# Kernel optimization log

Hardware: AMD Instinct MI355X
Metric: run time of the kernel (lower is better)

The kernel has to match this reference:

```python
import jax, jax.numpy as jnp
import numpy as np

E = 32      # feature/query dim
H = 4       # heads
HD = E // H # head dim = 8
N_LAYERS = 12
N_Q = 16
B = 128
S = 512


def _mha(q, kv, Wqkv, bqkv, Wo, bo):
    # PyTorch nn.MultiheadAttention (batch_first), eval mode (no dropout).
    Wq, Wk, Wv = jnp.split(Wqkv, 3, axis=0)   # each [E, E]
    bq, bk, bv = jnp.split(bqkv, 3)

    def heads(x, W, b):
        y = x @ W.T + b                         # [B, L, E]
        b_, l_, _ = y.shape
        return y.reshape(b_, l_, H, HD).transpose(0, 2, 1, 3)  # [B, H, L, HD]

    qh, kh, vh = heads(q, Wq, bq), heads(kv, Wk, bk), heads(kv, Wv, bv)
    scores = jnp.einsum('bhqd,bhkd->bhqk', qh, kh) / np.sqrt(HD).astype(np.float32)
    att = jax.nn.softmax(scores, axis=-1)
    o = jnp.einsum('bhqk,bhkd->bhqd', att, vh)
    o = o.transpose(0, 2, 1, 3).reshape(q.shape[0], q.shape[1], E)
    return o @ Wo.T + bo


def setup_inputs() -> dict:
    key = jax.random.key(0)
    ks = iter(jax.random.split(key, 64))
    g = lambda shape, s=0.05: (jax.random.normal(next(ks), shape, dtype=jnp.float32) * s)
    inp = {
        'x_omic': jax.random.normal(next(ks), (B, 80), dtype=jnp.float32),
        'x_path': jax.random.normal(next(ks), (B, S, E), dtype=jnp.float32),
        # frozen omic FFN encoder: 80 -> 64 -> 48 -> 32 -> 32, ELU each
        'omic_W0': g((64, 80)), 'omic_b0': g((64,)),
        'omic_W1': g((48, 64)), 'omic_b1': g((48,)),
        'omic_W2': g((32, 48)), 'omic_b2': g((32,)),
        'omic_W3': g((E, 32)),  'omic_b3': g((E,)),
        'ln_g': jnp.ones((E,), jnp.float32), 'ln_b': jnp.zeros((E,), jnp.float32),
        'corr_Wqkv': g((3 * E, E)), 'corr_bqkv': g((3 * E,)),
        'corr_Wo': g((E, E)), 'corr_bo': g((E,)),
        # 12 stacked query<->omic and query<->path cross-attentions
        'qo_Wqkv': g((N_LAYERS, 3 * E, E)), 'qo_bqkv': g((N_LAYERS, 3 * E)),
        'qo_Wo': g((N_LAYERS, E, E)), 'qo_bo': g((N_LAYERS, E)),
        'qp_Wqkv': g((N_LAYERS, 3 * E, E)), 'qp_bqkv': g((N_LAYERS, 3 * E)),
        'qp_Wo': g((N_LAYERS, E, E)), 'qp_bo': g((N_LAYERS, E)),
        # 12 stacked 2-layer FFNs (Linear-ReLU-Linear, no residual in source)
        'ffn_W1': g((N_LAYERS, E, E)), 'ffn_b1': g((N_LAYERS, E)),
        'ffn_W2': g((N_LAYERS, E, E)), 'ffn_b2': g((N_LAYERS, E)),
        'Qs': jax.random.normal(next(ks), (N_Q, E), dtype=jnp.float32),
        'grade_W': g((3, E)), 'grade_b': g((3,)),
        'haz_W': g((1, E)), 'haz_b': g((1,)),
    }
    return inp


def reference(x_omic, x_path, omic_W0, omic_b0, omic_W1, omic_b1, omic_W2, omic_b2,
              omic_W3, omic_b3, ln_g, ln_b, corr_Wqkv, corr_bqkv, corr_Wo, corr_bo,
              qo_Wqkv, qo_bqkv, qo_Wo, qo_bo, qp_Wqkv, qp_bqkv, qp_Wo, qp_bo,
              ffn_W1, ffn_b1, ffn_W2, ffn_b2, Qs, grade_W, grade_b, haz_W, haz_b):
    # frozen omic encoder (eval mode: AlphaDropout is identity)
    h = jax.nn.elu(x_omic @ omic_W0.T + omic_b0)
    h = jax.nn.elu(h @ omic_W1.T + omic_b1)
    h = jax.nn.elu(h @ omic_W2.T + omic_b2)
    omic_emb = jax.nn.elu(h @ omic_W3.T + omic_b3)[:, None, :]   # [B, 1, E]

    qs = jnp.broadcast_to(Qs[None], (x_omic.shape[0], N_Q, E))    # [B, 16, E]

    # correlation self-attention on LayerNorm(x_path), residual on raw x_path
    mu = jnp.mean(x_path, axis=-1, keepdims=True)
    var = jnp.var(x_path, axis=-1, keepdims=True)
    xn = (x_path - mu) / jnp.sqrt(var + 1e-5) * ln_g + ln_b
    img = x_path + _mha(xn, xn, corr_Wqkv, corr_bqkv, corr_Wo, corr_bo)

    for i in range(N_LAYERS):
        qs = _mha(qs, omic_emb, qo_Wqkv[i], qo_bqkv[i], qo_Wo[i], qo_bo[i])
        qs = _mha(qs, img, qp_Wqkv[i], qp_bqkv[i], qp_Wo[i], qp_bo[i])
        qs = jax.nn.relu(qs @ ffn_W1[i].T + ffn_b1[i]) @ ffn_W2[i].T + ffn_b2[i]

    features = qs.mean(axis=1)                                    # [B, E]
    grade = jax.nn.log_softmax(features @ grade_W.T + grade_b, axis=1)
    hazard = jax.nn.sigmoid(features @ haz_W.T + haz_b) * 6.0 - 3.0
    return features, grade, hazard
```

## Files before the change

### kernel.cpp

```cpp
#include <hip/hip_runtime.h>
#include <hip/hip_bf16.h>

typedef __attribute__((ext_vector_type(8))) short short8;
typedef __attribute__((ext_vector_type(4))) float f32x4;

__device__ __forceinline__ float elu1(float x) { return x > 0.f ? x : expm1f(x); }
__device__ __forceinline__ unsigned pkbf(float a, float b) {
  return (unsigned)__bfloat16_as_ushort(__float2bfloat16(a)) |
         ((unsigned)__bfloat16_as_ushort(__float2bfloat16(b)) << 16);
}
__device__ __forceinline__ short8 cvt8(float4 a, float4 b, float s) {
  uint4 u = { pkbf(a.x * s, a.y * s), pkbf(a.z * s, a.w * s),
              pkbf(b.x * s, b.y * s), pkbf(b.z * s, b.w * s) };
  union { uint4 u4; short8 s8; } c; c.u4 = u; return c.s8;
}
__device__ __forceinline__ unsigned pk_perm(float a, float b) {
  return __builtin_amdgcn_perm(__float_as_uint(b), __float_as_uint(a), 0x07060302u);
}

__global__ __launch_bounds__(512, 4) void k_fattn(
    const float* __restrict__ xp, const float* __restrict__ ln_g, const float* __restrict__ ln_b,
    const float* __restrict__ Wqkv, const float* __restrict__ bqkv,
    ushort* __restrict__ obf)
{
  __shared__ ushort qlds[512 * 8];
  __shared__ ushort klds[512 * 8];
  __shared__ ushort vts[8 * 512];
  __shared__ ushort ps[8][16 * 64];

  const float sc = 0.35355339059327373f * 1.4426950408889634f;
  int tid = threadIdx.x, w = tid >> 6, lane = tid & 63;
  int g = lane >> 4, qr = lane & 15;
  int bh = blockIdx.x, b = bh >> 2, h = bh & 3;
  const short8 z8 = {0, 0, 0, 0, 0, 0, 0, 0};

  int wrow = (qr < 8) ? (h * 8 + qr) : (32 + h * 8 + qr - 8);
  float qsc = (qr < 8) ? sc : 1.f;
  const float4* wr = (const float4*)(Wqkv + wrow * 32 + g * 8);
  short8 wqk = cvt8(wr[0], wr[1], qsc);
  short8 wv = z8;
  if (qr < 8) {
    const float4* vr = (const float4*)(Wqkv + (64 + h * 8 + qr) * 32 + g * 8);
    wv = cvt8(vr[0], vr[1], 1.f);
  }
  f32x4 bqk, bv;
  #pragma unroll
  for (int r = 0; r < 4; ++r) {
    bqk[r] = (g < 2) ? bqkv[h * 8 + g * 4 + r] * sc : bqkv[32 + h * 8 + (g - 2) * 4 + r];
    bv[r]  = (g < 2) ? bqkv[64 + h * 8 + g * 4 + r] : 0.f;
  }
  const float4* lg4 = (const float4*)(ln_g + g * 8);
  const float4* lb4 = (const float4*)(ln_b + g * 8);
  float4 ga = lg4[0], gb2 = lg4[1], ba = lb4[0], bb2 = lb4[1];

  #pragma unroll
  for (int i = 0; i < 4; ++i) {
    int rloc = w * 64 + i * 16 + qr;
    const float4* xr = (const float4*)(xp + (b * 512 + rloc) * 32 + g * 8);
    float4 x0 = xr[0], x1 = xr[1];
    float s1 = x0.x + x0.y + x0.z + x0.w + x1.x + x1.y + x1.z + x1.w;
    float s2 = x0.x*x0.x + x0.y*x0.y + x0.z*x0.z + x0.w*x0.w
             + x1.x*x1.x + x1.y*x1.y + x1.z*x1.z + x1.w*x1.w;
    s1 += __shfl_xor(s1, 16); s1 += __shfl_xor(s1, 32);
    s2 += __shfl_xor(s2, 16); s2 += __shfl_xor(s2, 32);
    float mu = s1 * 0.03125f;
    float rs = rsqrtf(s2 * 0.03125f - mu * mu + 1e-5f);
    float4 n0 = { (x0.x-mu)*rs*ga.x+ba.x, (x0.y-mu)*rs*ga.y+ba.y,
                  (x0.z-mu)*rs*ga.z+ba.z, (x0.w-mu)*rs*ga.w+ba.w };
    float4 n1 = { (x1.x-mu)*rs*gb2.x+bb2.x, (x1.y-mu)*rs*gb2.y+bb2.y,
                  (x1.z-mu)*rs*gb2.z+bb2.z, (x1.w-mu)*rs*gb2.w+bb2.w };
    short8 bx = cvt8(n0, n1, 1.f);

    f32x4 cqk = __builtin_amdgcn_mfma_f32_16x16x32_bf16(wqk, bx, bqk, 0, 0, 0);
    f32x4 cv  = __builtin_amdgcn_mfma_f32_16x16x32_bf16(wv,  bx, bv,  0, 0, 0);
    uint2 o2 = { pkbf(cqk[0], cqk[1]), pkbf(cqk[2], cqk[3]) };
    ushort* dst = (g < 2) ? qlds : klds;
    *(uint2*)(dst + rloc * 8 + (g & 1) * 4) = o2;
    if (g < 2) {
      #pragma unroll
      for (int r = 0; r < 4; ++r)
        vts[(g * 4 + r) * 512 + rloc] = __bfloat16_as_ushort(__float2bfloat16(cv[r]));
    }
  }
  __syncthreads();

  const short8 one8 = {(short)0x3F80, (short)0x3F80, (short)0x3F80, (short)0x3F80,
                       (short)0x3F80, (short)0x3F80, (short)0x3F80, (short)0x3F80};
  unsigned swz = (unsigned)(qr & 7) << 4;
  char* pw = (char*)&ps[w][0] + qr * 128;

  int qbase = w * 64;
  short8 qf0 = (g == 0) ? *(const short8*)(qlds + (qbase + qr) * 8) : z8;
  short8 qf1 = (g == 0) ? *(const short8*)(qlds + (qbase + 16 + qr) * 8) : z8;
  short8 qf2 = (g == 0) ? *(const short8*)(qlds + (qbase + 32 + qr) * 8) : z8;
  short8 qf3 = (g == 0) ? *(const short8*)(qlds + (qbase + 48 + qr) * 8) : z8;
  f32x4 ot0 = {0.f,0.f,0.f,0.f}, ot1 = {0.f,0.f,0.f,0.f};
  f32x4 ot2 = {0.f,0.f,0.f,0.f}, ot3 = {0.f,0.f,0.f,0.f};

#define QKPV(QF, OT) do {                                                       \
    _Pragma("unroll")                                                           \
    for (int t = 0; t < 4; ++t) {                                               \
      short8 af = *(const short8*)(kbase + t * 128);    \
      f32x4 s4 = __builtin_amdgcn_mfma_f32_16x16x32_bf16(af, QF,                \
                   (f32x4){0.f,0.f,0.f,0.f}, 0, 0, 0);                          \
      unsigned off = (unsigned)((t * 16 + g * 4) << 1) ^ swz;                   \
      uint2 pk2 = { pk_perm(__builtin_amdgcn_exp2f(s4[0]),                      \
                            __builtin_amdgcn_exp2f(s4[1])),                     \
                    pk_perm(__builtin_amdgcn_exp2f(s4[2]),                      \
                            __builtin_amdgcn_exp2f(s4[3])) };                   \
      *(uint2*)(pw + off) = pk2;                                                \
    }                                                                           \
    {                                                                           \
      short8 pb0 = *(const short8*)(pw + ((unsigned)((g * 8) << 1) ^ swz));     \
      OT = __builtin_amdgcn_mfma_f32_16x16x32_bf16(vf0, pb0, OT, 0, 0, 0);      \
      short8 pb1 = *(const short8*)(pw + ((unsigned)((32 + g * 8) << 1) ^ swz));\
      OT = __builtin_amdgcn_mfma_f32_16x16x32_bf16(vf1, pb1, OT, 0, 0, 0);      \
    }                                                                           \
  } while (0)

  for (int c = 0; c < 8; ++c) {
    const short8* vp = (const short8*)(vts + qr * 512 + c * 64 + g * 8);
    short8 vf0 = (qr < 8) ? vp[0] : one8;
    short8 vf1 = (qr < 8) ? vp[4] : one8;
    const ushort* kbase = klds + c * 64 * 8 + qr * 8;
    QKPV(qf0, ot0);
    QKPV(qf1, ot1);
    QKPV(qf2, ot2);
    QKPV(qf3, ot3);
  }
#undef QKPV

  #pragma unroll
  for (int i = 0; i < 4; ++i) {
    f32x4 ot = (i == 0) ? ot0 : (i == 1) ? ot1 : (i == 2) ? ot2 : ot3;
    float lpv = __shfl(ot[0], 32 + qr, 64);
    float rl = 1.f / lpv;
    if (g < 2) {
      int rowg = bh * 512 + qbase + i * 16 + qr;
      uint2 o2 = { pkbf(ot[0] * rl, ot[1] * rl), pkbf(ot[2] * rl, ot[3] * rl) };
      *(uint2*)((unsigned*)obf + rowg * 4 + g * 2) = o2;
    }
  }
}

__global__ __launch_bounds__(512) void k_final(
    const ushort* __restrict__ obf, const float* __restrict__ xp,
    const float* __restrict__ Wo, const float* __restrict__ bo,
    const float* __restrict__ xo,
    const float* __restrict__ oW0, const float* __restrict__ ob0,
    const float* __restrict__ oW1, const float* __restrict__ ob1,
    const float* __restrict__ oW2, const float* __restrict__ ob2,
    const float* __restrict__ oW3, const float* __restrict__ ob3,
    const float* __restrict__ qoW, const float* __restrict__ qob,
    const float* __restrict__ qoWo, const float* __restrict__ qobo,
    const float* __restrict__ qpW, const float* __restrict__ qpb,
    const float* __restrict__ qpWo, const float* __restrict__ qpbo,
    const float* __restrict__ fW1, const float* __restrict__ fb1,
    const float* __restrict__ fW2, const float* __restrict__ fb2,
    const float* __restrict__ gW, const float* __restrict__ gb,
    const float* __restrict__ hW, const float* __restrict__ hb,
    float* __restrict__ out)
{
  __shared__ float4 imgl[512 * 8];
  __shared__ float p[4][512];
  __shared__ float partial[16][4][32];
  __shared__ float buf1[80], buf2[64];
  __shared__ float emb[32], qbar[32], qh[32], u[4][32], cc4[4], lsum[4], ctx4[4][32], t32[32], o32[32];
  int b = blockIdx.x, tid = threadIdx.x;
  int w = tid >> 6, lane = tid & 63, g = lane >> 4, qr = lane & 15;

  {
    short8 wa[2]; f32x4 bc2[2];
    #pragma unroll
    for (int t = 0; t < 2; ++t) {
      const float4* wrr = (const float4*)(Wo + (t * 16 + qr) * 32 + g * 8);
      wa[t] = cvt8(wrr[0], wrr[1], 1.f);
      const float4 bb = *(const float4*)(bo + t * 16 + g * 4);
      bc2[t] = (f32x4){bb.x, bb.y, bb.z, bb.w};
    }
    #pragma unroll
    for (int j = 0; j < 4; ++j) {
      int rloc = j * 128 + w * 16 + qr;
      short8 ob = *(const short8*)(obf + ((b * 4 + g) * 512 + rloc) * 8);
      #pragma unroll
      for (int t = 0; t < 2; ++t) {
        f32x4 ct = __builtin_amdgcn_mfma_f32_16x16x32_bf16(wa[t], ob, bc2[t], 0, 0, 0);
        int e4 = t * 4 + g;
        float4 xv = *(const float4*)(xp + (b * 512 + rloc) * 32 + e4 * 4);
        imgl[rloc * 8 + (e4 ^ (rloc & 7))] =
            (float4){ xv.x + ct[0], xv.y + ct[1], xv.z + ct[2], xv.w + ct[3] };
      }
    }
  }
  __syncthreads();

  if (tid < 80) buf1[tid] = xo[b * 80 + tid];
  __syncthreads();
  if (tid < 64) { float a = ob0[tid]; const float* wgt = oW0 + tid * 80;
    for (int e = 0; e < 80; ++e) a += buf1[e] * wgt[e]; buf2[tid] = elu1(a); }
  __syncthreads();
  if (tid < 48) { float a = ob1[tid]; const float* wgt = oW1 + tid * 64;
    for (int e = 0; e < 64; ++e) a += buf2[e] * wgt[e]; buf1[tid] = elu1(a); }
  __syncthreads();
  if (tid < 32) { float a = ob2[tid]; const float* wgt = oW2 + tid * 48;
    for (int e = 0; e < 48; ++e) a += buf1[e] * wgt[e]; buf2[tid] = elu1(a); }
  __syncthreads();
  if (tid < 32) { float a = ob3[tid]; const float* wgt = oW3 + tid * 32;
    for (int e = 0; e < 32; ++e) a += buf2[e] * wgt[e]; emb[tid] = elu1(a); }
  __syncthreads();

  if (tid < 32) { float a = qob[64 + tid]; const float* wgt = qoW + (64 + tid) * 32;
    for (int e = 0; e < 32; ++e) a += emb[e] * wgt[e]; t32[tid] = a; }
  __syncthreads();
  if (tid < 32) { float a = qobo[tid]; const float* wgt = qoWo + tid * 32;
    for (int e = 0; e < 32; ++e) a += t32[e] * wgt[e]; qbar[tid] = a; }
  __syncthreads();

  if (tid < 32) { float a = qpb[tid]; const float* wgt = qpW + tid * 32;
    for (int e = 0; e < 32; ++e) a += qbar[e] * wgt[e]; qh[tid] = a; }
  __syncthreads();
  if (tid < 128) {
    int hh = tid >> 5, e = tid & 31;
    float a = 0.f;
    #pragma unroll
    for (int d = 0; d < 8; ++d) a += qh[hh * 8 + d] * qpW[(32 + hh * 8 + d) * 32 + e];
    u[hh][e] = a;
    if (e == 0) { float c2 = 0.f; for (int d = 0; d < 8; ++d) c2 += qh[hh * 8 + d] * qpb[32 + hh * 8 + d]; cc4[hh] = c2; }
  }
  __syncthreads();

  #pragma unroll
  for (int j = 0; j < 4; ++j) {
    int idx = tid + j * 512; int hh = idx >> 9, kk = idx & 511;
    const float* uh = u[hh];
    float a = cc4[hh];
    #pragma unroll
    for (int e4 = 0; e4 < 8; ++e4) {
      float4 t = imgl[kk * 8 + (e4 ^ (kk & 7))];
      a += uh[e4 * 4] * t.x + uh[e4 * 4 + 1] * t.y + uh[e4 * 4 + 2] * t.z + uh[e4 * 4 + 3] * t.w;
    }
    p[hh][kk] = __builtin_amdgcn_exp2f(fminf(a * 0.51006979f, 115.f));
  }
  __syncthreads();
  if (tid < 256) {
    int ww = tid >> 6, ln2 = tid & 63;
    float a = 0.f;
    for (int kk = ln2; kk < 512; kk += 64) a += p[ww][kk];
    #pragma unroll
    for (int m = 32; m >= 1; m >>= 1) a += __shfl_xor(a, m, 64);
    if (ln2 == 0) lsum[ww] = 1.f / a;
  }
  {
    int e = tid & 31, ch = tid >> 5;
    float a0 = 0.f, a1 = 0.f, a2 = 0.f, a3 = 0.f;
    for (int kk = ch * 32; kk < ch * 32 + 32; ++kk) {
      float val = ((const float*)&imgl[kk * 8 + ((e >> 2) ^ (kk & 7))])[e & 3];
      a0 += p[0][kk] * val; a1 += p[1][kk] * val; a2 += p[2][kk] * val; a3 += p[3][kk] * val;
    }
    partial[ch][0][e] = a0; partial[ch][1][e] = a1; partial[ch][2][e] = a2; partial[ch][3][e] = a3;
  }
  __syncthreads();
  if (tid < 128) {
    int hh = tid >> 5, e = tid & 31;
    float a = 0.f;
    #pragma unroll
    for (int ch = 0; ch < 16; ++ch) a += partial[ch][hh][e];
    ctx4[hh][e] = a * lsum[hh];
  }
  __syncthreads();
  if (tid < 32) { int hh = tid >> 3;
    float a = qpb[64 + tid]; const float* wgt = qpW + (64 + tid) * 32;
    for (int e = 0; e < 32; ++e) a += ctx4[hh][e] * wgt[e]; o32[tid] = a; }
  __syncthreads();
  if (tid < 32) { float a = qpbo[tid]; const float* wgt = qpWo + tid * 32;
    for (int e = 0; e < 32; ++e) a += o32[e] * wgt[e]; t32[tid] = a; }
  __syncthreads();

  if (tid < 32) { float a = fb1[tid]; const float* wgt = fW1 + tid * 32;
    for (int e = 0; e < 32; ++e) a += t32[e] * wgt[e]; o32[tid] = fmaxf(a, 0.f); }
  __syncthreads();
  if (tid < 32) { float a = fb2[tid]; const float* wgt = fW2 + tid * 32;
    for (int e = 0; e < 32; ++e) a += o32[e] * wgt[e]; qbar[tid] = a; }
  __syncthreads();

  if (tid < 32) out[b * 32 + tid] = qbar[tid];
  if (tid == 0) {
    float g0 = gb[0], g1 = gb[1], g2 = gb[2];
    for (int e = 0; e < 32; ++e) { float f = qbar[e]; g0 += f * gW[e]; g1 += f * gW[32 + e]; g2 += f * gW[64 + e]; }
    float m = fmaxf(g0, fmaxf(g1, g2));
    float lse = m + logf(expf(g0 - m) + expf(g1 - m) + expf(g2 - m));
    float* og = out + 4096;
    og[b * 3 + 0] = g0 - lse; og[b * 3 + 1] = g1 - lse; og[b * 3 + 2] = g2 - lse;
    float hz = hb[0];
    for (int e = 0; e < 32; ++e) hz += qbar[e] * hW[e];
    out[4480 + b] = 1.f / (1.f + expf(-hz)) * 6.f - 3.f;
  }
}

extern "C" void kernel_launch(void* const* d_in, const int* in_sizes, int n_in,
                              void* d_out, int out_size, void* d_ws, size_t ws_size,
                              hipStream_t stream) {
  const float* x_omic = (const float*)d_in[0];
  const float* x_path = (const float*)d_in[1];
  const float* oW0 = (const float*)d_in[2];  const float* ob0 = (const float*)d_in[3];
  const float* oW1 = (const float*)d_in[4];  const float* ob1 = (const float*)d_in[5];
  const float* oW2 = (const float*)d_in[6];  const float* ob2 = (const float*)d_in[7];
  const float* oW3 = (const float*)d_in[8];  const float* ob3 = (const float*)d_in[9];
  const float* ln_g = (const float*)d_in[10]; const float* ln_b = (const float*)d_in[11];
  const float* cW  = (const float*)d_in[12]; const float* cb  = (const float*)d_in[13];
  const float* cWo = (const float*)d_in[14]; const float* cbo = (const float*)d_in[15];
  const float* qoW = (const float*)d_in[16]; const float* qob = (const float*)d_in[17];
  const float* qoWo = (const float*)d_in[18]; const float* qobo = (const float*)d_in[19];
  const float* qpW = (const float*)d_in[20]; const float* qpb = (const float*)d_in[21];
  const float* qpWo = (const float*)d_in[22]; const float* qpbo = (const float*)d_in[23];
  const float* fW1 = (const float*)d_in[24]; const float* fb1 = (const float*)d_in[25];
  const float* fW2 = (const float*)d_in[26]; const float* fb2 = (const float*)d_in[27];
  const float* gW = (const float*)d_in[29]; const float* gb = (const float*)d_in[30];
  const float* hW = (const float*)d_in[31]; const float* hb = (const float*)d_in[32];

  float* out = (float*)d_out;
  ushort* obf = (ushort*)d_ws;

  const int L = 11;
  k_fattn<<<512, 512, 0, stream>>>(x_path, ln_g, ln_b, cW, cb, obf);
  k_final<<<128, 512, 0, stream>>>(obf, x_path, cWo, cbo, x_omic,
      oW0, ob0, oW1, ob1, oW2, ob2, oW3, ob3,
      qoW + L * 96 * 32, qob + L * 96, qoWo + L * 32 * 32, qobo + L * 32,
      qpW + L * 96 * 32, qpb + L * 96, qpWo + L * 32 * 32, qpbo + L * 32,
      fW1 + L * 32 * 32, fb1 + L * 32, fW2 + L * 32 * 32, fb2 + L * 32,
      gW, gb, hW, hb, out);
}
```

Before: 49.77 us.

## Switch flash attention to 32x32x16 MFMA with permlane32 swap instead of LDS P staging

Rewrites the attention inner loop to use 32x32x16 bf16 MFMA tiles, with 32 queries and 32 keys per step. The exponentiated score fragment is rearranged into the B-operand layout in registers using permlane32_swap, which removes the per-wave shared-memory P buffer, its stores and reloads, and the swizzle logic. The row-sum trick (a ones row in V) now sits at row 8 of the 32-row output. The cost is more accumulator registers per wave and a layout that relies on the permlane32_swap instruction, which is only available on newer CDNA parts.

```diff
diff --git a/kernel.cpp b/kernel.cpp
--- a/kernel.cpp
+++ b/kernel.cpp
@@ -3,6 +3,8 @@
 
 typedef __attribute__((ext_vector_type(8))) short short8;
 typedef __attribute__((ext_vector_type(4))) float f32x4;
+typedef __attribute__((ext_vector_type(16))) float f32x16;
+typedef __attribute__((ext_vector_type(2))) unsigned uint2e;
 
 __device__ __forceinline__ float elu1(float x) { return x > 0.f ? x : expm1f(x); }
 __device__ __forceinline__ unsigned pkbf(float a, float b) {
@@ -26,7 +28,6 @@
   __shared__ ushort qlds[512 * 8];
   __shared__ ushort klds[512 * 8];
   __shared__ ushort vts[8 * 512];
-  __shared__ ushort ps[8][16 * 64];
 
   const float sc = 0.35355339059327373f * 1.4426950408889634f;
   int tid = threadIdx.x, w = tid >> 6, lane = tid & 63;
@@ -86,60 +87,51 @@
 
   const short8 one8 = {(short)0x3F80, (short)0x3F80, (short)0x3F80, (short)0x3F80,
                        (short)0x3F80, (short)0x3F80, (short)0x3F80, (short)0x3F80};
-  unsigned swz = (unsigned)(qr & 7) << 4;
-  char* pw = (char*)&ps[w][0] + qr * 128;
-
-  int qbase = w * 64;
-  short8 qf0 = (g == 0) ? *(const short8*)(qlds + (qbase + qr) * 8) : z8;
-  short8 qf1 = (g == 0) ? *(const short8*)(qlds + (qbase + 16 + qr) * 8) : z8;
-  short8 qf2 = (g == 0) ? *(const short8*)(qlds + (qbase + 32 + qr) * 8) : z8;
-  short8 qf3 = (g == 0) ? *(const short8*)(qlds + (qbase + 48 + qr) * 8) : z8;
-  f32x4 ot0 = {0.f,0.f,0.f,0.f}, ot1 = {0.f,0.f,0.f,0.f};
-  f32x4 ot2 = {0.f,0.f,0.f,0.f}, ot3 = {0.f,0.f,0.f,0.f};
-
-#define QKPV(QF, OT) do {                                                       \
-    _Pragma("unroll")                                                           \
-    for (int t = 0; t < 4; ++t) {                                               \
-      short8 af = *(const short8*)(kbase + t * 128);    \
-      f32x4 s4 = __builtin_amdgcn_mfma_f32_16x16x32_bf16(af, QF,                \
-                   (f32x4){0.f,0.f,0.f,0.f}, 0, 0, 0);                          \
-      unsigned off = (unsigned)((t * 16 + g * 4) << 1) ^ swz;                   \
-      uint2 pk2 = { pk_perm(__builtin_amdgcn_exp2f(s4[0]),                      \
-                            __builtin_amdgcn_exp2f(s4[1])),                     \
-                    pk_perm(__builtin_amdgcn_exp2f(s4[2]),                      \
-                            __builtin_amdgcn_exp2f(s4[3])) };                   \
-      *(uint2*)(pw + off) = pk2;                                                \
-    }                                                                           \
-    {                                                                           \
-      short8 pb0 = *(const short8*)(pw + ((unsigned)((g * 8) << 1) ^ swz));     \
-      OT = __builtin_amdgcn_mfma_f32_16x16x32_bf16(vf0, pb0, OT, 0, 0, 0);      \
-      short8 pb1 = *(const short8*)(pw + ((unsigned)((32 + g * 8) << 1) ^ swz));\
-      OT = __builtin_amdgcn_mfma_f32_16x16x32_bf16(vf1, pb1, OT, 0, 0, 0);      \
-    }                                                                           \
+  const f32x16 z16 = {};
+  int half = lane >> 5, lq = lane & 31;
+
+  short8 qfA = (half == 0) ? *(const short8*)(qlds + (w * 64 + lq) * 8) : z8;
+  short8 qfB = (half == 0) ? *(const short8*)(qlds + (w * 64 + 32 + lq) * 8) : z8;
+  f32x16 accA = {}, accB = {};
+
+#define QSTEP(QF, ACC) do {                                                          \
+    f32x16 s = __builtin_amdgcn_mfma_f32_32x32x16_bf16(kf, QF, z16, 0, 0, 0);        \
+    unsigned w0 = pk_perm(__builtin_amdgcn_exp2f(s[0]),  __builtin_amdgcn_exp2f(s[1]));  \
+    unsigned w1 = pk_perm(__builtin_amdgcn_exp2f(s[2]),  __builtin_amdgcn_exp2f(s[3]));  \
+    unsigned w2 = pk_perm(__builtin_amdgcn_exp2f(s[4]),  __builtin_amdgcn_exp2f(s[5]));  \
+    unsigned w3 = pk_perm(__builtin_amdgcn_exp2f(s[6]),  __builtin_amdgcn_exp2f(s[7]));  \
+    unsigned w4 = pk_perm(__builtin_amdgcn_exp2f(s[8]),  __builtin_amdgcn_exp2f(s[9]));  \
+    unsigned w5 = pk_perm(__builtin_amdgcn_exp2f(s[10]), __builtin_amdgcn_exp2f(s[11])); \
+    unsigned w6 = pk_perm(__builtin_amdgcn_exp2f(s[12]), __builtin_amdgcn_exp2f(s[13])); \
+    unsigned w7 = pk_perm(__builtin_amdgcn_exp2f(s[14]), __builtin_amdgcn_exp2f(s[15])); \
+    uint2e r02 = __builtin_amdgcn_permlane32_swap(w0, w2, false, false);             \
+    uint2e r13 = __builtin_amdgcn_permlane32_swap(w1, w3, false, false);             \
+    uint2e r46 = __builtin_amdgcn_permlane32_swap(w4, w6, false, false);             \
+    uint2e r57 = __builtin_amdgcn_permlane32_swap(w5, w7, false, false);             \
+    union { uint4 u; short8 s8; } pA, pB;                                            \
+    pA.u = (uint4){r02.x, r13.x, r02.y, r13.y};                                      \
+    pB.u = (uint4){r46.x, r57.x, r46.y, r57.y};                                      \
+    ACC = __builtin_amdgcn_mfma_f32_32x32x16_bf16(vfA, pA.s8, ACC, 0, 0, 0);         \
+    ACC = __builtin_amdgcn_mfma_f32_32x32x16_bf16(vfB, pB.s8, ACC, 0, 0, 0);         \
   } while (0)
 
-  for (int c = 0; c < 8; ++c) {
-    const short8* vp = (const short8*)(vts + qr * 512 + c * 64 + g * 8);
-    short8 vf0 = (qr < 8) ? vp[0] : one8;
-    short8 vf1 = (qr < 8) ? vp[4] : one8;
-    const ushort* kbase = klds + c * 64 * 8 + qr * 8;
-    QKPV(qf0, ot0);
-    QKPV(qf1, ot1);
-    QKPV(qf2, ot2);
-    QKPV(qf3, ot3);
-  }
-#undef QKPV
+  for (int c = 0; c < 16; ++c) {
+    short8 kf = (half == 0) ? *(const short8*)(klds + (c * 32 + lq) * 8) : z8;
+    const ushort* vbase = vts + lq * 512 + c * 32 + half * 8;
+    short8 vfA = (lq < 8) ? *(const short8*)(vbase)      : (lq == 8 ? one8 : z8);
+    short8 vfB = (lq < 8) ? *(const short8*)(vbase + 16) : (lq == 8 ? one8 : z8);
+    QSTEP(qfA, accA);
+    QSTEP(qfB, accB);
+  }
+#undef QSTEP
 
   #pragma unroll
-  for (int i = 0; i < 4; ++i) {
-    f32x4 ot = (i == 0) ? ot0 : (i == 1) ? ot1 : (i == 2) ? ot2 : ot3;
-    float lpv = __shfl(ot[0], 32 + qr, 64);
-    float rl = 1.f / lpv;
-    if (g < 2) {
-      int rowg = bh * 512 + qbase + i * 16 + qr;
-      uint2 o2 = { pkbf(ot[0] * rl, ot[1] * rl), pkbf(ot[2] * rl, ot[3] * rl) };
-      *(uint2*)((unsigned*)obf + rowg * 4 + g * 2) = o2;
-    }
+  for (int qs = 0; qs < 2; ++qs) {
+    f32x16 acc = qs ? accB : accA;
+    float rl = 1.f / __shfl(acc[4], lq, 64);
+    int rowg = bh * 512 + w * 64 + qs * 32 + lq;
+    uint2 o2 = { pkbf(acc[0] * rl, acc[1] * rl), pkbf(acc[2] * rl, acc[3] * rl) };
+    *(uint2*)((unsigned*)obf + rowg * 4 + half * 2) = o2;
   }
 }
 
```

Measured after the change: 47.29 us (median of 2 runs). -5.0%, faster.
